# Kernel tuning notes

Measured on AMD Instinct MI355X. Metric: run time of the kernel, lower is better.

## Reference

```python
import jax, jax.numpy as jnp
import numpy as np
import math

B, N, D, H = 256, 2048, 128, 8
HD = D // H  # 16
TANH_CLIP = 10.0
TEMP = 1.0


def setup_inputs() -> dict:
    key = jax.random.key(0)
    ks = jax.random.split(key, 10)
    context_node_projected = jax.random.normal(ks[0], (B, 1, D), dtype=jnp.float32)
    node_embeddings = jax.random.normal(ks[1], (B, N, D), dtype=jnp.float32)
    glimpse_K = jax.random.normal(ks[2], (H, B, 1, N, HD), dtype=jnp.float32)
    glimpse_V = jax.random.normal(ks[3], (H, B, 1, N, HD), dtype=jnp.float32)
    logit_K = jax.random.normal(ks[4], (B, 1, N, D), dtype=jnp.float32)
    W_ctx = jax.random.normal(ks[5], (2 * D, D), dtype=jnp.float32) * 0.05
    W_out = jax.random.normal(ks[6], (D, D), dtype=jnp.float32) * 0.05
    first_a = jax.random.randint(ks[7], (B, 1), 0, N, dtype=jnp.int32)
    current_node = jax.random.randint(ks[8], (B, 1), 0, N, dtype=jnp.int32)
    mask = jax.random.uniform(ks[9], (B, 1, N)) < 0.3
    mask = mask.at[:, :, 0].set(False)  # guarantee at least one feasible node
    return {
        "context_node_projected": context_node_projected,
        "node_embeddings": node_embeddings,
        "glimpse_K": glimpse_K,
        "glimpse_V": glimpse_V,
        "logit_K": logit_K,
        "W_ctx": W_ctx,
        "W_out": W_out,
        "first_a": first_a,
        "current_node": current_node,
        "mask": mask,
    }


def reference(context_node_projected, node_embeddings, glimpse_K, glimpse_V,
              logit_K, W_ctx, W_out, first_a, current_node, mask):
    # --- step context: gather first and current node embeddings (i > 0 branch) ---
    idx = jnp.concatenate([first_a, current_node], axis=1)          # [B, 2]
    ctx = jnp.take_along_axis(node_embeddings, idx[:, :, None], axis=1)  # [B, 2, D]
    ctx = ctx.reshape(ctx.shape[0], 1, 2 * ctx.shape[-1])           # [B, 1, 2D]
    query = context_node_projected + ctx @ W_ctx                    # [B, 1, D]

    b, steps, d = query.shape
    # glimpse_Q: [H, B, steps, 1, HD]
    glimpse_Q = query.reshape(b, steps, H, 1, HD).transpose(2, 0, 1, 3, 4)
    # compatibility: [H, B, steps, 1, N]
    compat = jnp.matmul(glimpse_Q, jnp.swapaxes(glimpse_K, -2, -1)) / math.sqrt(HD)
    # inner mask: masked positions -> -inf before softmax
    compat = jnp.where(mask[None, :, :, None, :], -jnp.inf, compat)
    attn = jax.nn.softmax(compat, axis=-1)                          # [H, B, steps, 1, N]
    heads = jnp.matmul(attn, glimpse_V)                             # [H, B, steps, 1, HD]
    # concat heads -> [B, steps, 1, D], then project_out
    heads = heads.transpose(1, 2, 3, 0, 4).reshape(b, steps, 1, H * HD)
    glimpse = heads @ W_out                                         # final_Q: [B, steps, 1, D]
    # logit attention against logit_K: [B, steps, N]
    logits = jnp.matmul(glimpse, jnp.swapaxes(logit_K, -2, -1)).squeeze(-2) / math.sqrt(d)
    logits = jnp.tanh(logits) * TANH_CLIP
    logits = jnp.where(mask, -jnp.inf, logits)
    log_p = jax.nn.log_softmax(logits / TEMP, axis=-1)              # [B, steps, N]
    return log_p
```

## Files before the change

kernel.cpp:

```cpp
#include <hip/hip_runtime.h>
#include <math.h>

#define BB 256
#define NN 2048
#define DD 128
#define HH 8
#define HDD 16

#define WSQ_OFF 0
#define WSA_OFF 32768
#define WSL_OFF 114688

typedef float v4f __attribute__((ext_vector_type(4)));

__device__ __forceinline__ v4f ntload4(const float* p) {
    return __builtin_nontemporal_load((const v4f*)p);
}

__global__ __launch_bounds__(128) void k_query(
    const float* __restrict__ ctxproj, const float* __restrict__ node_emb,
    const float* __restrict__ Wctx, const int* __restrict__ first_a,
    const int* __restrict__ cur_node, float* __restrict__ wsq)
{
    const int b = blockIdx.x, d = threadIdx.x;
    __shared__ float s_ctx[2*DD];
    const int i0 = first_a[b], i1 = cur_node[b];
    s_ctx[d]      = node_emb[((size_t)b*NN + i0)*DD + d];
    s_ctx[d + DD] = node_emb[((size_t)b*NN + i1)*DD + d];
    __syncthreads();
    float q = ctxproj[(size_t)b*DD + d];
    #pragma unroll 8
    for (int k = 0; k < 2*DD; ++k)
        q = fmaf(s_ctx[k], Wctx[(size_t)k*DD + d], q);
    wsq[(size_t)b*DD + d] = q;
}

__global__ __launch_bounds__(256, 6) void k_attn(
    const float* __restrict__ gK, const float* __restrict__ gV,
    const unsigned char* __restrict__ mask, const float* __restrict__ wsq,
    float* __restrict__ wsa)
{
    const int bid  = blockIdx.x;
    const int b    = bid >> 4;
    const int h    = (bid >> 1) & 7;
    const int half = bid & 1;
    const int tid  = threadIdx.x;
    const int lane = tid & 63;
    const int w    = tid >> 6;
    const int qq   = tid >> 2;
    const int sub  = tid & 3;

    __shared__ unsigned char s_codeT[1024];
    __shared__ float s_q[HDD];
    __shared__ float s_m[4];
    __shared__ float s_red[4][1 + HDD];

    {
        const unsigned int mm =
            ((const unsigned int*)(mask + (size_t)b*NN + half*1024))[tid];
        const unsigned int m0 = (mm & 0x000000ffu) ? 1u : 0u;
        const unsigned int m1 = (mm & 0x0000ff00u) ? 1u : 0u;
        const unsigned int m2 = (mm & 0x00ff0000u) ? 1u : 0u;
        const unsigned int m3 = (mm & 0xff000000u) ? 1u : 0u;
        const unsigned int l01 = m0 & m1, l23 = m2 & m3;
        const int n0 = tid * 4;
        s_codeT[((n0+0)&63)*16 + ((n0+0)>>6)] = (unsigned char)(m0 | (l01<<1));
        s_codeT[((n0+1)&63)*16 + ((n0+1)>>6)] = (unsigned char)(m1 | (l01<<1));
        s_codeT[((n0+2)&63)*16 + ((n0+2)>>6)] = (unsigned char)(m2 | (l23<<1));
        s_codeT[((n0+3)&63)*16 + ((n0+3)>>6)] = (unsigned char)(m3 | (l23<<1));
    }
    if (tid < HDD) s_q[tid] = wsq[(size_t)b*DD + h*HDD + tid];
    __syncthreads();

    float q4[4];
    #pragma unroll
    for (int j = 0; j < 4; ++j) q4[j] = s_q[sub*4 + j];

    unsigned int cw[4];
    #pragma unroll
    for (int t = 0; t < 4; ++t)
        cw[t] = ((const unsigned int*)(s_codeT + qq*16))[t];

    const float* __restrict__ Kh =
        gK + ((size_t)(h*BB + b))*NN*HDD + (size_t)half*1024*HDD;
    const float* __restrict__ Vh =
        gV + ((size_t)(h*BB + b))*NN*HDD + (size_t)half*1024*HDD;

    float c[16];
    #pragma unroll
    for (int i = 0; i < 16; ++i) {
        const unsigned int code = (cw[i>>2] >> (8*(i&3))) & 3u;
        const int ro = i*1024 + ((code & 2u) ? sub*4 : tid*4);
        const v4f kv = ntload4(Kh + ro);
        float d;
        d = kv.x * q4[0];
        d = fmaf(kv.y, q4[1], d);
        d = fmaf(kv.z, q4[2], d);
        d = fmaf(kv.w, q4[3], d);
        c[i] = d;
    }
    #pragma unroll
    for (int i = 0; i < 16; ++i) c[i] += __shfl_xor(c[i], 1);
    #pragma unroll
    for (int i = 0; i < 16; ++i) c[i] += __shfl_xor(c[i], 2);
    #pragma unroll
    for (int i = 0; i < 16; ++i) {
        const unsigned int code = (cw[i>>2] >> (8*(i&3))) & 3u;
        c[i] = (code & 1u) ? -1e30f : c[i] * 0.25f;
    }

    float m = c[0];
    #pragma unroll
    for (int i = 1; i < 16; ++i) m = fmaxf(m, c[i]);
    #pragma unroll
    for (int off = 4; off < 64; off <<= 1) m = fmaxf(m, __shfl_xor(m, off));
    if (lane == 0) s_m[w] = m;
    __syncthreads();
    m = fmaxf(fmaxf(s_m[0], s_m[1]), fmaxf(s_m[2], s_m[3]));

    float s = 0.f;
    float a4[4] = {0.f, 0.f, 0.f, 0.f};
    #pragma unroll
    for (int i = 0; i < 16; ++i) {
        const unsigned int code = (cw[i>>2] >> (8*(i&3))) & 3u;
        const int ro = i*1024 + ((code & 2u) ? sub*4 : tid*4);
        const v4f vv = ntload4(Vh + ro);
        const float p = expf(c[i] - m);
        s += p;
        a4[0] = fmaf(p, vv.x, a4[0]);
        a4[1] = fmaf(p, vv.y, a4[1]);
        a4[2] = fmaf(p, vv.z, a4[2]);
        a4[3] = fmaf(p, vv.w, a4[3]);
    }

    #pragma unroll
    for (int off = 4; off < 64; off <<= 1) {
        s += __shfl_xor(s, off);
        #pragma unroll
        for (int j = 0; j < 4; ++j) a4[j] += __shfl_xor(a4[j], off);
    }
    if (lane < 4) {
        if (lane == 0) s_red[w][0] = s;
        #pragma unroll
        for (int j = 0; j < 4; ++j) s_red[w][1 + lane*4 + j] = a4[j];
    }
    __syncthreads();

    float* __restrict__ wp = wsa + ((size_t)(b*HH + h)*2 + half)*20;
    if (w == 0 && lane < HDD)
        wp[2 + lane] = s_red[0][1+lane] + s_red[1][1+lane]
                     + s_red[2][1+lane] + s_red[3][1+lane];
    if (tid == 0) {
        wp[0] = m;
        wp[1] = s_red[0][0] + s_red[1][0] + s_red[2][0] + s_red[3][0];
    }
}

__global__ __launch_bounds__(256, 6) void k_logits(
    const float* __restrict__ lK, const float* __restrict__ Wout,
    const unsigned char* __restrict__ mask, const float* __restrict__ wsa,
    float* __restrict__ out_tv, float* __restrict__ wsp)
{
    const int bid  = blockIdx.x;
    const int b    = bid >> 3;
    const int seg  = bid & 7;
    const int tid  = threadIdx.x;
    const int lane = tid & 63;
    const int w    = tid >> 6;
    const int rg   = lane >> 2;
    const int sub  = lane & 3;

    __shared__ float s_h[DD];
    __shared__ float s_part[2][DD];
    __shared__ float s_g[DD];
    __shared__ unsigned char s_mk[256];
    __shared__ float s_tv[256];
    __shared__ float s_rm[4];
    __shared__ float s_rs[4];

    if (tid < DD) {
        const int h = tid >> 4, j = tid & 15;
        const float* p1 = wsa + (size_t)(b*HH + h)*40;
        const float* p2 = p1 + 20;
        const float m1 = p1[0], s1 = p1[1], a1 = p1[2+j];
        const float m2 = p2[0], s2 = p2[1], a2 = p2[2+j];
        const float ms = fmaxf(m1, m2);
        const float e1 = expf(m1 - ms), e2 = expf(m2 - ms);
        s_h[tid] = (a1*e1 + a2*e2) / (s1*e1 + s2*e2);
    }
    if (tid < 64)
        ((unsigned int*)s_mk)[tid] =
            ((const unsigned int*)(mask + (size_t)b*NN + (seg << 8)))[tid];
    __syncthreads();

    {
        const int d = tid & 127, hf = tid >> 7, k0 = hf * 64;
        float a = 0.f;
        #pragma unroll 8
        for (int k = 0; k < 64; ++k)
            a = fmaf(s_h[k0 + k], Wout[(size_t)(k0 + k)*DD + d], a);
        s_part[hf][d] = a;
    }
    __syncthreads();
    if (tid < DD) s_g[tid] = s_part[0][tid] + s_part[1][tid];
    __syncthreads();

    float gr[32];
    #pragma unroll
    for (int j = 0; j < 8; ++j)
        #pragma unroll
        for (int t = 0; t < 4; ++t)
            gr[j*4 + t] = s_g[j*16 + sub*4 + t];

    const float* __restrict__ base = lK + ((size_t)b*NN + (seg << 8))*DD;

    #pragma unroll
    for (int it = 0; it < 4; ++it) {
        const int rl = it*64 + w*16 + rg;
        const bool mk = s_mk[rl] != 0;
        const size_t ro = mk ? 0 : (size_t)rl * DD;
        float dot = 0.f;
        #pragma unroll
        for (int j = 0; j < 8; ++j) {
            const float4 f = *(const float4*)(base + ro + j*16 + sub*4);
            dot = fmaf(f.x, gr[j*4+0], dot);
            dot = fmaf(f.y, gr[j*4+1], dot);
            dot = fmaf(f.z, gr[j*4+2], dot);
            dot = fmaf(f.w, gr[j*4+3], dot);
        }
        dot += __shfl_xor(dot, 1);
        dot += __shfl_xor(dot, 2);
        if (sub == 0)
            s_tv[rl] = mk ? -1e30f : tanhf(dot * 0.088388347648318447f) * 10.f;
    }
    __syncthreads();

    const float tv = s_tv[tid];
    float m = tv;
    #pragma unroll
    for (int off = 1; off < 64; off <<= 1) m = fmaxf(m, __shfl_xor(m, off));
    if (lane == 0) s_rm[w] = m;
    __syncthreads();
    const float bm = fmaxf(fmaxf(s_rm[0], s_rm[1]), fmaxf(s_rm[2], s_rm[3]));
    float e = expf(tv - bm);
    #pragma unroll
    for (int off = 1; off < 64; off <<= 1) e += __shfl_xor(e, off);
    if (lane == 0) s_rs[w] = e;
    __syncthreads();
    if (tid == 0)
        { wsp[(size_t)bid*2] = bm;
          wsp[(size_t)bid*2 + 1] = s_rs[0] + s_rs[1] + s_rs[2] + s_rs[3]; }

    out_tv[(size_t)b*NN + (seg << 8) + tid] = tv;
}

__global__ __launch_bounds__(256) void k_final(
    const unsigned char* __restrict__ mask, const float* __restrict__ wsp,
    float* __restrict__ out)
{
    const int bid = blockIdx.x;
    const int b   = bid >> 3;
    const int seg = bid & 7;
    const int tid = threadIdx.x;
    __shared__ float s_p[16];
    if (tid < 16) s_p[tid] = wsp[(size_t)b*16 + tid];
    __syncthreads();
    float mstar = -1e30f;
    #pragma unroll
    for (int i = 0; i < 8; ++i) mstar = fmaxf(mstar, s_p[2*i]);
    float ss = 0.f;
    #pragma unroll
    for (int i = 0; i < 8; ++i) ss += s_p[2*i+1] * expf(s_p[2*i] - mstar);
    const float lse = mstar + logf(ss);

    const size_t idx = (size_t)b*NN + (seg << 8) + tid;
    const float tv = out[idx];
    out[idx] = mask[idx] ? -1e30f : tv - lse;
}

extern "C" void kernel_launch(void* const* d_in, const int* in_sizes, int n_in,
                              void* d_out, int out_size, void* d_ws, size_t ws_size,
                              hipStream_t stream) {
    const float* ctxproj  = (const float*)d_in[0];
    const float* node_emb = (const float*)d_in[1];
    const float* gK       = (const float*)d_in[2];
    const float* gV       = (const float*)d_in[3];
    const float* lK       = (const float*)d_in[4];
    const float* Wctx     = (const float*)d_in[5];
    const float* Wout     = (const float*)d_in[6];
    const int*   first_a  = (const int*)d_in[7];
    const int*   cur_node = (const int*)d_in[8];
    const unsigned char* mask = (const unsigned char*)d_in[9];
    float* out = (float*)d_out;
    float* ws  = (float*)d_ws;

    float* wsq = ws + WSQ_OFF;
    float* wsa = ws + WSA_OFF;
    float* wsp = ws + WSL_OFF;

    hipLaunchKernelGGL(k_query,  dim3(BB),       dim3(128), 0, stream,
                       ctxproj, node_emb, Wctx, first_a, cur_node, wsq);
    hipLaunchKernelGGL(k_attn,   dim3(BB*HH*2),  dim3(256), 0, stream,
                       gK, gV, mask, wsq, wsa);
    hipLaunchKernelGGL(k_logits, dim3(BB*8),     dim3(256), 0, stream,
                       lK, Wout, mask, wsa, out, wsp);
    hipLaunchKernelGGL(k_final,  dim3(BB*8),     dim3(256), 0, stream,
                       mask, wsp, out);
}
```

Baseline: 143.0 us.

## Fuse query projection into attention kernel and split N into quarters

Removes the separate k_query launch by computing each head's 16-dim query slice inside k_attn from the gathered node embeddings and W_ctx. The attention grid is split four ways over N instead of two, giving more blocks with fewer loads per thread, and k_logits now merges four partial softmax states. The cost is redundant query computation across the 4 quarter-blocks of each head, plus extra syncs and shared memory per block.

```diff
diff --git a/kernel.cpp b/kernel.cpp
--- a/kernel.cpp
+++ b/kernel.cpp
@@ -7,9 +7,8 @@
 #define HH 8
 #define HDD 16
 
-#define WSQ_OFF 0
-#define WSA_OFF 32768
-#define WSL_OFF 114688
+#define WSA_OFF 0
+#define WSL_OFF 163840
 
 typedef float v4f __attribute__((ext_vector_type(4)));
 
@@ -17,78 +16,87 @@
     return __builtin_nontemporal_load((const v4f*)p);
 }
 
-__global__ __launch_bounds__(128) void k_query(
+__global__ __launch_bounds__(256, 6) void k_attn(
+    const float* __restrict__ gK, const float* __restrict__ gV,
+    const unsigned char* __restrict__ mask,
     const float* __restrict__ ctxproj, const float* __restrict__ node_emb,
     const float* __restrict__ Wctx, const int* __restrict__ first_a,
-    const int* __restrict__ cur_node, float* __restrict__ wsq)
-{
-    const int b = blockIdx.x, d = threadIdx.x;
-    __shared__ float s_ctx[2*DD];
-    const int i0 = first_a[b], i1 = cur_node[b];
-    s_ctx[d]      = node_emb[((size_t)b*NN + i0)*DD + d];
-    s_ctx[d + DD] = node_emb[((size_t)b*NN + i1)*DD + d];
-    __syncthreads();
-    float q = ctxproj[(size_t)b*DD + d];
-    #pragma unroll 8
-    for (int k = 0; k < 2*DD; ++k)
-        q = fmaf(s_ctx[k], Wctx[(size_t)k*DD + d], q);
-    wsq[(size_t)b*DD + d] = q;
-}
-
-__global__ __launch_bounds__(256, 6) void k_attn(
-    const float* __restrict__ gK, const float* __restrict__ gV,
-    const unsigned char* __restrict__ mask, const float* __restrict__ wsq,
+    const int* __restrict__ cur_node,
     float* __restrict__ wsa)
 {
     const int bid  = blockIdx.x;
-    const int b    = bid >> 4;
-    const int h    = (bid >> 1) & 7;
-    const int half = bid & 1;
+    const int b    = bid >> 5;
+    const int h    = (bid >> 2) & 7;
+    const int qt   = bid & 3;
     const int tid  = threadIdx.x;
     const int lane = tid & 63;
     const int w    = tid >> 6;
     const int qq   = tid >> 2;
     const int sub  = tid & 3;
 
-    __shared__ unsigned char s_codeT[1024];
+    __shared__ unsigned char s_codeT[512];
+    __shared__ float s_ctx[2*DD];
+    __shared__ float s_qp[16][17];
     __shared__ float s_q[HDD];
     __shared__ float s_m[4];
     __shared__ float s_red[4][1 + HDD];
 
     {
+        const int i0 = first_a[b], i1 = cur_node[b];
+        s_ctx[tid] = (tid < DD)
+            ? node_emb[((size_t)b*NN + i0)*DD + tid]
+            : node_emb[((size_t)b*NN + i1)*DD + (tid - DD)];
+    }
+    if (tid < 128) {
         const unsigned int mm =
-            ((const unsigned int*)(mask + (size_t)b*NN + half*1024))[tid];
+            ((const unsigned int*)(mask + (size_t)b*NN + qt*512))[tid];
         const unsigned int m0 = (mm & 0x000000ffu) ? 1u : 0u;
         const unsigned int m1 = (mm & 0x0000ff00u) ? 1u : 0u;
         const unsigned int m2 = (mm & 0x00ff0000u) ? 1u : 0u;
         const unsigned int m3 = (mm & 0xff000000u) ? 1u : 0u;
         const unsigned int l01 = m0 & m1, l23 = m2 & m3;
         const int n0 = tid * 4;
-        s_codeT[((n0+0)&63)*16 + ((n0+0)>>6)] = (unsigned char)(m0 | (l01<<1));
-        s_codeT[((n0+1)&63)*16 + ((n0+1)>>6)] = (unsigned char)(m1 | (l01<<1));
-        s_codeT[((n0+2)&63)*16 + ((n0+2)>>6)] = (unsigned char)(m2 | (l23<<1));
-        s_codeT[((n0+3)&63)*16 + ((n0+3)>>6)] = (unsigned char)(m3 | (l23<<1));
-    }
-    if (tid < HDD) s_q[tid] = wsq[(size_t)b*DD + h*HDD + tid];
+        s_codeT[((n0+0)&63)*8 + ((n0+0)>>6)] = (unsigned char)(m0 | (l01<<1));
+        s_codeT[((n0+1)&63)*8 + ((n0+1)>>6)] = (unsigned char)(m1 | (l01<<1));
+        s_codeT[((n0+2)&63)*8 + ((n0+2)>>6)] = (unsigned char)(m2 | (l23<<1));
+        s_codeT[((n0+3)&63)*8 + ((n0+3)>>6)] = (unsigned char)(m3 | (l23<<1));
+    }
+    __syncthreads();
+
+    {
+        const int j = tid & 15, kc = tid >> 4;
+        float a = 0.f;
+        #pragma unroll
+        for (int k = 0; k < 16; ++k)
+            a = fmaf(s_ctx[kc*16 + k],
+                     Wctx[(size_t)(kc*16 + k)*DD + h*HDD + j], a);
+        s_qp[kc][j] = a;
+    }
+    __syncthreads();
+    if (tid < HDD) {
+        float a = ctxproj[(size_t)b*DD + h*HDD + tid];
+        #pragma unroll
+        for (int kc = 0; kc < 16; ++kc) a += s_qp[kc][tid];
+        s_q[tid] = a;
+    }
     __syncthreads();
 
     float q4[4];
     #pragma unroll
     for (int j = 0; j < 4; ++j) q4[j] = s_q[sub*4 + j];
 
-    unsigned int cw[4];
-    #pragma unroll
-    for (int t = 0; t < 4; ++t)
-        cw[t] = ((const unsigned int*)(s_codeT + qq*16))[t];
+    unsigned int cw[2];
+    cw[0] = ((const unsigned int*)(s_codeT + qq*8))[0];
+    cw[1] = ((const unsigned int*)(s_codeT + qq*8))[1];
 
     const float* __restrict__ Kh =
-        gK + ((size_t)(h*BB + b))*NN*HDD + (size_t)half*1024*HDD;
+        gK + ((size_t)(h*BB + b))*NN*HDD + (size_t)qt*512*HDD;
     const float* __restrict__ Vh =
-        gV + ((size_t)(h*BB + b))*NN*HDD + (size_t)half*1024*HDD;
-
-    float c[16];
-    #pragma unroll
-    for (int i = 0; i < 16; ++i) {
+        gV + ((size_t)(h*BB + b))*NN*HDD + (size_t)qt*512*HDD;
+
+    float c[8];
+    #pragma unroll
+    for (int i = 0; i < 8; ++i) {
         const unsigned int code = (cw[i>>2] >> (8*(i&3))) & 3u;
         const int ro = i*1024 + ((code & 2u) ? sub*4 : tid*4);
         const v4f kv = ntload4(Kh + ro);
@@ -100,18 +108,18 @@
         c[i] = d;
     }
     #pragma unroll
-    for (int i = 0; i < 16; ++i) c[i] += __shfl_xor(c[i], 1);
-    #pragma unroll
-    for (int i = 0; i < 16; ++i) c[i] += __shfl_xor(c[i], 2);
-    #pragma unroll
-    for (int i = 0; i < 16; ++i) {
+    for (int i = 0; i < 8; ++i) c[i] += __shfl_xor(c[i], 1);
+    #pragma unroll
+    for (int i = 0; i < 8; ++i) c[i] += __shfl_xor(c[i], 2);
+    #pragma unroll
+    for (int i = 0; i < 8; ++i) {
         const unsigned int code = (cw[i>>2] >> (8*(i&3))) & 3u;
         c[i] = (code & 1u) ? -1e30f : c[i] * 0.25f;
     }
 
     float m = c[0];
     #pragma unroll
-    for (int i = 1; i < 16; ++i) m = fmaxf(m, c[i]);
+    for (int i = 1; i < 8; ++i) m = fmaxf(m, c[i]);
     #pragma unroll
     for (int off = 4; off < 64; off <<= 1) m = fmaxf(m, __shfl_xor(m, off));
     if (lane == 0) s_m[w] = m;
@@ -121,7 +129,7 @@
     float s = 0.f;
     float a4[4] = {0.f, 0.f, 0.f, 0.f};
     #pragma unroll
-    for (int i = 0; i < 16; ++i) {
+    for (int i = 0; i < 8; ++i) {
         const unsigned int code = (cw[i>>2] >> (8*(i&3))) & 3u;
         const int ro = i*1024 + ((code & 2u) ? sub*4 : tid*4);
         const v4f vv = ntload4(Vh + ro);
@@ -146,7 +154,7 @@
     }
     __syncthreads();
 
-    float* __restrict__ wp = wsa + ((size_t)(b*HH + h)*2 + half)*20;
+    float* __restrict__ wp = wsa + ((size_t)((b*HH + h)*4 + qt))*20;
     if (w == 0 && lane < HDD)
         wp[2 + lane] = s_red[0][1+lane] + s_red[1][1+lane]
                      + s_red[2][1+lane] + s_red[3][1+lane];
@@ -180,13 +188,19 @@
 
     if (tid < DD) {
         const int h = tid >> 4, j = tid & 15;
-        const float* p1 = wsa + (size_t)(b*HH + h)*40;
-        const float* p2 = p1 + 20;
-        const float m1 = p1[0], s1 = p1[1], a1 = p1[2+j];
-        const float m2 = p2[0], s2 = p2[1], a2 = p2[2+j];
-        const float ms = fmaxf(m1, m2);
-        const float e1 = expf(m1 - ms), e2 = expf(m2 - ms);
-        s_h[tid] = (a1*e1 + a2*e2) / (s1*e1 + s2*e2);
+        const float* p0 = wsa + ((size_t)(b*HH + h)*4)*20;
+        float m = p0[0], s = p0[1], a = p0[2+j];
+        #pragma unroll
+        for (int qt = 1; qt < 4; ++qt) {
+            const float* pq = p0 + qt*20;
+            const float m2 = pq[0], s2 = pq[1], a2 = pq[2+j];
+            const float mn = fmaxf(m, m2);
+            const float e1 = expf(m - mn), e2 = expf(m2 - mn);
+            s = s*e1 + s2*e2;
+            a = a*e1 + a2*e2;
+            m = mn;
+        }
+        s_h[tid] = a / s;
     }
     if (tid < 64)
         ((unsigned int*)s_mk)[tid] =
@@ -294,14 +308,12 @@
     float* out = (float*)d_out;
     float* ws  = (float*)d_ws;
 
-    float* wsq = ws + WSQ_OFF;
     float* wsa = ws + WSA_OFF;
     float* wsp = ws + WSL_OFF;
 
-    hipLaunchKernelGGL(k_query,  dim3(BB),       dim3(128), 0, stream,
-                       ctxproj, node_emb, Wctx, first_a, cur_node, wsq);
-    hipLaunchKernelGGL(k_attn,   dim3(BB*HH*2),  dim3(256), 0, stream,
-                       gK, gV, mask, wsq, wsa);
+    hipLaunchKernelGGL(k_attn,   dim3(BB*HH*4),  dim3(256), 0, stream,
+                       gK, gV, mask, ctxproj, node_emb, Wctx,
+                       first_a, cur_node, wsa);
     hipLaunchKernelGGL(k_logits, dim3(BB*8),     dim3(256), 0, stream,
                        lK, Wout, mask, wsa, out, wsp);
     hipLaunchKernelGGL(k_final,  dim3(BB*8),     dim3(256), 0, stream,
```

New measurement: 131.7 us. -7.9%, faster.
